# Optimization experiments

Hardware: AMD Instinct MI355X
Metric: run time of the kernel (lower is better)

## Reference

```python
import jax, jax.numpy as jnp
import numpy as np

D = 1024
H = 16
HD = D // H
FF = 4096
B = 4
S = 1024
EPS = 1e-5


def layer_norm(x, g, b):
    mu = jnp.mean(x, axis=-1, keepdims=True)
    var = jnp.mean(jnp.square(x - mu), axis=-1, keepdims=True)
    return (x - mu) * jax.lax.rsqrt(var + EPS) * g + b


def setup_inputs() -> dict:
    key = jax.random.key(0)
    ks = jax.random.split(key, 16)
    s = 0.02
    return {
        "src": jax.random.normal(ks[0], (B, S, D), jnp.float32),
        "attn_bias": jax.random.normal(ks[1], (H, S, S), jnp.float32),
        "Wqkv": jax.random.normal(ks[2], (3 * D, D), jnp.float32) * s,
        "bqkv": jnp.zeros((3 * D,), jnp.float32),
        "Wo": jax.random.normal(ks[3], (D, D), jnp.float32) * s,
        "bo": jnp.zeros((D,), jnp.float32),
        "g1": jnp.ones((D,), jnp.float32),
        "b1n": jnp.zeros((D,), jnp.float32),
        "g2": jnp.ones((D,), jnp.float32),
        "b2n": jnp.zeros((D,), jnp.float32),
        "W1": jax.random.normal(ks[4], (FF, D), jnp.float32) * s,
        "b1": jnp.zeros((FF,), jnp.float32),
        "W2": jax.random.normal(ks[5], (D, FF), jnp.float32) * s,
        "b2": jnp.zeros((D,), jnp.float32),
    }


def reference(src, attn_bias, Wqkv, bqkv, Wo, bo, g1, b1n, g2, b2n, W1, b1, W2, b2):
    bsz, seq, _ = src.shape
    qkv = src @ Wqkv.T + bqkv                      # [B,S,3D]
    q, k, v = jnp.split(qkv, 3, axis=-1)
    q = q.reshape(bsz, seq, H, HD)
    k = k.reshape(bsz, seq, H, HD)
    v = v.reshape(bsz, seq, H, HD)
    scores = jnp.einsum('bthd,bshd->bhts', q, k) / np.sqrt(HD).astype(np.float32)
    scores = scores + attn_bias[None]              # 3D bias broadcast over batch
    w = jax.nn.softmax(scores, axis=-1)
    ctx = jnp.einsum('bhts,bshd->bthd', w, v).reshape(bsz, seq, D)
    attn_out = ctx @ Wo.T + bo
    x = layer_norm(src + attn_out, g1, b1n)
    ff = (jax.nn.gelu(x @ W1.T + b1, approximate=False)) @ W2.T + b2
    return layer_norm(x + ff, g2, b2n)
```

## Files before the change

kernel.cpp:

```cpp
#include <hip/hip_runtime.h>
#include <cstdint>

typedef unsigned short u16;
typedef __bf16 bf16x8 __attribute__((ext_vector_type(8)));
typedef float f32x4 __attribute__((ext_vector_type(4)));
typedef unsigned short u16x8 __attribute__((ext_vector_type(8)));
typedef unsigned short u16x4 __attribute__((ext_vector_type(4)));

__device__ __forceinline__ u16 f2b(float f) {
  union { float f; unsigned u; } x; x.f = f;
  unsigned r = (x.u + 0x7FFFu + ((x.u >> 16) & 1u)) >> 16;
  return (u16)r;
}
__device__ __forceinline__ float b2f(u16 v) {
  union { unsigned u; float f; } x; x.u = (unsigned)v << 16; return x.f;
}

__device__ __forceinline__ void gload_lds16(const void* g, void* l) {
  __builtin_amdgcn_global_load_lds(
      (__attribute__((address_space(1))) void*)(uintptr_t)g,
      (__attribute__((address_space(3))) void*)(uintptr_t)l, 16, 0, 0);
}

struct CastArgs {
  const float* in[5];
  u16* out[5];
  int cum[6];
};
__global__ void cast_multi(CastArgs a) {
  const int i = blockIdx.x * 256 + threadIdx.x;
  int r = 0;
#pragma unroll
  for (int k = 1; k < 5; ++k) r += (i >= a.cum[k]);
  const int local = i - a.cum[r];
  const float4 v = *(const float4*)(a.in[r] + (size_t)local * 4);
  u16x4 o = {f2b(v.x), f2b(v.y), f2b(v.z), f2b(v.w)};
  *(u16x4*)(a.out[r] + (size_t)local * 4) = o;
}

template<bool GELU_ACT, bool WRITE_VT>
__global__ void gemm_nt(const u16* __restrict__ A, const u16* __restrict__ Bw,
                        const float* __restrict__ bias, u16* __restrict__ Cb,
                        u16* __restrict__ Vt, int M, int N, int K) {
  __shared__ u16 As[2][128 * 32];
  __shared__ u16 Bs[2][128 * 32];
  const int tid = threadIdx.x;
  const int lane = tid & 63, wid = tid >> 6;
  const int bm = blockIdx.y * 128, bn = blockIdx.x * 128;
  const int wm = wid >> 1, wn = wid & 1;
  const int r = lane & 15, g = lane >> 4;
  const int s4 = (r >> 1) & 3;

  auto stage = [&](int buf, int k0) {
#pragma unroll
    for (int i = 0; i < 2; ++i) {
      const int c = tid + i * 256;
      const int row = c >> 2, ch = c & 3;
      const int gs = ch ^ ((row >> 1) & 3);
      gload_lds16(A + (size_t)(bm + row) * K + k0 + gs * 8, &As[buf][c * 8]);
      gload_lds16(Bw + (size_t)(bn + row) * K + k0 + gs * 8, &Bs[buf][c * 8]);
    }
  };

  f32x4 acc[4][4] = {};
  stage(0, 0);
  __syncthreads();
  const int nk = K >> 5;
  int cur = 0;
  for (int kt = 0; kt < nk; ++kt) {
    if (kt + 1 < nk) stage(cur ^ 1, (kt + 1) * 32);
    bf16x8 af[4], bfr[4];
#pragma unroll
    for (int m = 0; m < 4; ++m)
      af[m] = *(const bf16x8*)&As[cur][(wm * 64 + m * 16 + r) * 32 + (g ^ s4) * 8];
#pragma unroll
    for (int n = 0; n < 4; ++n)
      bfr[n] = *(const bf16x8*)&Bs[cur][(wn * 64 + n * 16 + r) * 32 + (g ^ s4) * 8];
#pragma unroll
    for (int m = 0; m < 4; ++m)
#pragma unroll
      for (int n = 0; n < 4; ++n)
        acc[m][n] = __builtin_amdgcn_mfma_f32_16x16x32_bf16(af[m], bfr[n], acc[m][n], 0, 0, 0);
    __syncthreads();
    cur ^= 1;
  }
#pragma unroll
  for (int m = 0; m < 4; ++m) {
    const int row0 = bm + wm * 64 + m * 16 + g * 4;
#pragma unroll
    for (int n = 0; n < 4; ++n) {
      const int col = bn + wn * 64 + n * 16 + r;
      const float bv = bias[col];
      if (WRITE_VT && col >= 2048) {
        const int hv = col - 2048;
        const int bb = row0 >> 10, s0 = row0 & 1023;
        u16x4 ov;
#pragma unroll
        for (int j = 0; j < 4; ++j) ov[j] = f2b(acc[m][n][j] + bv);
        *(u16x4*)(Vt + (((size_t)(bb * 16 + (hv >> 6))) * 64 + (hv & 63)) * 1024 + s0) = ov;
      } else {
#pragma unroll
        for (int j = 0; j < 4; ++j) {
          float v = acc[m][n][j] + bv;
          if (GELU_ACT) v = 0.5f * v * (1.f + erff(v * 0.70710678118654752f));
          Cb[(size_t)(row0 + j) * N + col] = f2b(v);
        }
      }
    }
  }
}

__global__ void gemm_nt_splitk(const u16* __restrict__ A, const u16* __restrict__ Bw,
                               float* __restrict__ parts, int M, int N, int K, int Kc) {
  __shared__ u16 As[2][128 * 32];
  __shared__ u16 Bs[2][128 * 32];
  const int tid = threadIdx.x;
  const int lane = tid & 63, wid = tid >> 6;
  const int bm = blockIdx.y * 128, bn = blockIdx.x * 128;
  const int kbase = blockIdx.z * Kc;
  const int wm = wid >> 1, wn = wid & 1;
  const int r = lane & 15, g = lane >> 4;
  const int s4 = (r >> 1) & 3;

  auto stage = [&](int buf, int k0) {
#pragma unroll
    for (int i = 0; i < 2; ++i) {
      const int c = tid + i * 256;
      const int row = c >> 2, ch = c & 3;
      const int gs = ch ^ ((row >> 1) & 3);
      gload_lds16(A + (size_t)(bm + row) * K + k0 + gs * 8, &As[buf][c * 8]);
      gload_lds16(Bw + (size_t)(bn + row) * K + k0 + gs * 8, &Bs[buf][c * 8]);
    }
  };

  f32x4 acc[4][4] = {};
  stage(0, kbase);
  __syncthreads();
  const int nk = Kc >> 5;
  int cur = 0;
  for (int kt = 0; kt < nk; ++kt) {
    if (kt + 1 < nk) stage(cur ^ 1, kbase + (kt + 1) * 32);
    bf16x8 af[4], bfr[4];
#pragma unroll
    for (int m = 0; m < 4; ++m)
      af[m] = *(const bf16x8*)&As[cur][(wm * 64 + m * 16 + r) * 32 + (g ^ s4) * 8];
#pragma unroll
    for (int n = 0; n < 4; ++n)
      bfr[n] = *(const bf16x8*)&Bs[cur][(wn * 64 + n * 16 + r) * 32 + (g ^ s4) * 8];
#pragma unroll
    for (int m = 0; m < 4; ++m)
#pragma unroll
      for (int n = 0; n < 4; ++n)
        acc[m][n] = __builtin_amdgcn_mfma_f32_16x16x32_bf16(af[m], bfr[n], acc[m][n], 0, 0, 0);
    __syncthreads();
    cur ^= 1;
  }
  float* Cp = parts + (size_t)blockIdx.z * M * N;
#pragma unroll
  for (int m = 0; m < 4; ++m) {
    const int row0 = bm + wm * 64 + m * 16 + g * 4;
#pragma unroll
    for (int n = 0; n < 4; ++n) {
      const int col = bn + wn * 64 + n * 16 + r;
#pragma unroll
      for (int j = 0; j < 4; ++j)
        Cp[(size_t)(row0 + j) * N + col] = acc[m][n][j];
    }
  }
}

__global__ __launch_bounds__(256) void attn_kernel(
    const u16* __restrict__ qkv, const u16* __restrict__ Vt,
    const float* __restrict__ bias, u16* __restrict__ ctx) {
  const int yy = blockIdx.y;
  const int h = yy >> 2, b = yy & 3;
  const int q0 = blockIdx.x * 32;
  const int tid = threadIdx.x;
  const int lane = tid & 63, wid = tid >> 6;
  const int r = lane & 15, g = lane >> 4;
  const int bh = b * 16 + h;

  __shared__ __align__(16) u16 PB[2][16 * 1024];

  const size_t qb0 = (size_t)(b * 1024 + q0 + r) * 3072 + h * 64;
  const size_t qb1 = (size_t)(b * 1024 + q0 + 16 + r) * 3072 + h * 64;
  const bf16x8 aq00 = *(const bf16x8*)(qkv + qb0 + g * 8);
  const bf16x8 aq01 = *(const bf16x8*)(qkv + qb0 + 32 + g * 8);
  const bf16x8 aq10 = *(const bf16x8*)(qkv + qb1 + g * 8);
  const bf16x8 aq11 = *(const bf16x8*)(qkv + qb1 + 32 + g * 8);

  const int n0 = wid * 256;
  const float* brow0 = bias + ((size_t)h * 1024 + q0 + r) * 1024;
  const float* brow1 = brow0 + 16 * 1024;

#pragma unroll 4
  for (int nt = 0; nt < 16; ++nt) {
    const int key = n0 + nt * 16 + r;
    const size_t kbase = (size_t)(b * 1024 + key) * 3072 + 1024 + h * 64;
    const bf16x8 bk0 = *(const bf16x8*)(qkv + kbase + g * 8);
    const bf16x8 bk1 = *(const bf16x8*)(qkv + kbase + 32 + g * 8);
    const int col = n0 + nt * 16 + g * 4;
    const float4 bb0 = *(const float4*)(brow0 + col);
    const float4 bb1 = *(const float4*)(brow1 + col);
    f32x4 a0 = {0.f, 0.f, 0.f, 0.f}, a1 = {0.f, 0.f, 0.f, 0.f};
    a0 = __builtin_amdgcn_mfma_f32_16x16x32_bf16(bk0, aq00, a0, 0, 0, 0);
    a1 = __builtin_amdgcn_mfma_f32_16x16x32_bf16(bk0, aq10, a1, 0, 0, 0);
    a0 = __builtin_amdgcn_mfma_f32_16x16x32_bf16(bk1, aq01, a0, 0, 0, 0);
    a1 = __builtin_amdgcn_mfma_f32_16x16x32_bf16(bk1, aq11, a1, 0, 0, 0);
    const int idx = r * 1024 + (col ^ ((r & 15) << 3));
    u16x4 o0 = {f2b(fmaf(a0[0], 0.125f, bb0.x)), f2b(fmaf(a0[1], 0.125f, bb0.y)),
                f2b(fmaf(a0[2], 0.125f, bb0.z)), f2b(fmaf(a0[3], 0.125f, bb0.w))};
    u16x4 o1 = {f2b(fmaf(a1[0], 0.125f, bb1.x)), f2b(fmaf(a1[1], 0.125f, bb1.y)),
                f2b(fmaf(a1[2], 0.125f, bb1.z)), f2b(fmaf(a1[3], 0.125f, bb1.w))};
    *(u16x4*)&PB[0][idx] = o0;
    *(u16x4*)&PB[1][idx] = o1;
  }
  __syncthreads();

#pragma unroll
  for (int tr = 0; tr < 8; ++tr) {
    const int t = tr & 1, rr = tr >> 1;
    const int row = wid * 4 + rr;
    const int swz = (row & 15) << 3;
    u16* prow = &PB[t][row * 1024];
    const int c0 = lane * 16;
    const u16x8 v0 = *(const u16x8*)&prow[c0 ^ swz];
    const u16x8 v1 = *(const u16x8*)&prow[(c0 + 8) ^ swz];
    float f[16];
#pragma unroll
    for (int k = 0; k < 8; ++k) { f[k] = b2f(v0[k]); f[8 + k] = b2f(v1[k]); }
    float m = f[0];
#pragma unroll
    for (int k = 1; k < 16; ++k) m = fmaxf(m, f[k]);
    m = fmaxf(m, __shfl_xor(m, 1));  m = fmaxf(m, __shfl_xor(m, 2));
    m = fmaxf(m, __shfl_xor(m, 4));  m = fmaxf(m, __shfl_xor(m, 8));
    m = fmaxf(m, __shfl_xor(m, 16)); m = fmaxf(m, __shfl_xor(m, 32));
    float s = 0.f;
#pragma unroll
    for (int k = 0; k < 16; ++k) { f[k] = __expf(f[k] - m); s += f[k]; }
    s += __shfl_xor(s, 1);  s += __shfl_xor(s, 2);
    s += __shfl_xor(s, 4);  s += __shfl_xor(s, 8);
    s += __shfl_xor(s, 16); s += __shfl_xor(s, 32);
    const float inv = 1.f / s;
    u16x8 o0, o1;
#pragma unroll
    for (int k = 0; k < 8; ++k) {
      o0[k] = f2b(f[k] * inv);
      o1[k] = f2b(f[8 + k] * inv);
    }
    *(u16x8*)&prow[c0 ^ swz] = o0;
    *(u16x8*)&prow[(c0 + 8) ^ swz] = o1;
  }
  __syncthreads();

  f32x4 oa = {0.f, 0.f, 0.f, 0.f}, ob = {0.f, 0.f, 0.f, 0.f};
  const u16* vrow = Vt + ((size_t)bh * 64 + wid * 16 + r) * 1024;
#pragma unroll 4
  for (int ks = 0; ks < 32; ++ks) {
    const int off = (ks * 32 + g * 8) ^ ((r & 15) << 3);
    const bf16x8 vb = *(const bf16x8*)(vrow + ks * 32 + g * 8);
    const bf16x8 pa0 = *(const bf16x8*)&PB[0][r * 1024 + off];
    const bf16x8 pa1 = *(const bf16x8*)&PB[1][r * 1024 + off];
    oa = __builtin_amdgcn_mfma_f32_16x16x32_bf16(pa0, vb, oa, 0, 0, 0);
    ob = __builtin_amdgcn_mfma_f32_16x16x32_bf16(pa1, vb, ob, 0, 0, 0);
  }
#pragma unroll
  for (int j = 0; j < 4; ++j) {
    ctx[(size_t)(b * 1024 + q0 + g * 4 + j) * 1024 + h * 64 + wid * 16 + r] = f2b(oa[j]);
    ctx[(size_t)(b * 1024 + q0 + 16 + g * 4 + j) * 1024 + h * 64 + wid * 16 + r] = f2b(ob[j]);
  }
}

template<int NP>
__global__ void ln_sum_kernel(const float* __restrict__ parts,
                              const float* __restrict__ resid,
                              const float* __restrict__ cbias,
                              const float* __restrict__ gw, const float* __restrict__ bw,
                              float* __restrict__ outf, u16* __restrict__ outb) {
  const int row = blockIdx.x, tid = threadIdx.x;
  const size_t off = (size_t)row * 1024 + tid * 4;
  float4 v = *(const float4*)(resid + off);
  const float4 cb = *(const float4*)(cbias + tid * 4);
  v.x += cb.x; v.y += cb.y; v.z += cb.z; v.w += cb.w;
#pragma unroll
  for (int p = 0; p < NP; ++p) {
    const float4 a = *(const float4*)(parts + (size_t)p * 4096 * 1024 + off);
    v.x += a.x; v.y += a.y; v.z += a.z; v.w += a.w;
  }
  float s = v.x + v.y + v.z + v.w;
  float q = v.x * v.x + v.y * v.y + v.z * v.z + v.w * v.w;
#pragma unroll
  for (int m = 32; m >= 1; m >>= 1) { s += __shfl_xor(s, m); q += __shfl_xor(q, m); }
  __shared__ float rs[4], rq[4];
  if ((tid & 63) == 0) { rs[tid >> 6] = s; rq[tid >> 6] = q; }
  __syncthreads();
  s = rs[0] + rs[1] + rs[2] + rs[3];
  q = rq[0] + rq[1] + rq[2] + rq[3];
  const float mu = s * (1.f / 1024.f);
  const float inv = rsqrtf(q * (1.f / 1024.f) - mu * mu + 1e-5f);
  const float4 g4 = *(const float4*)(gw + tid * 4);
  const float4 b4 = *(const float4*)(bw + tid * 4);
  float4 o;
  o.x = (v.x - mu) * inv * g4.x + b4.x;
  o.y = (v.y - mu) * inv * g4.y + b4.y;
  o.z = (v.z - mu) * inv * g4.z + b4.z;
  o.w = (v.w - mu) * inv * g4.w + b4.w;
  if (outf) *(float4*)(outf + off) = o;
  if (outb) {
    u16x4 ob = {f2b(o.x), f2b(o.y), f2b(o.z), f2b(o.w)};
    *(u16x4*)(outb + off) = ob;
  }
}

extern "C" void kernel_launch(void* const* d_in, const int* in_sizes, int n_in,
                              void* d_out, int out_size, void* d_ws, size_t ws_size,
                              hipStream_t stream) {
  (void)in_sizes; (void)n_in; (void)out_size; (void)ws_size;
  const float* src   = (const float*)d_in[0];
  const float* abias = (const float*)d_in[1];
  const float* Wqkv  = (const float*)d_in[2];
  const float* bqkv  = (const float*)d_in[3];
  const float* Wo    = (const float*)d_in[4];
  const float* bo    = (const float*)d_in[5];
  const float* g1    = (const float*)d_in[6];
  const float* b1n   = (const float*)d_in[7];
  const float* g2    = (const float*)d_in[8];
  const float* b2n   = (const float*)d_in[9];
  const float* W1    = (const float*)d_in[10];
  const float* b1    = (const float*)d_in[11];
  const float* W2    = (const float*)d_in[12];
  const float* b2    = (const float*)d_in[13];
  float* out = (float*)d_out;

  char* ws = (char*)d_ws;
  const size_t MB = 1024 * 1024;
  u16* srcb  = (u16*)(ws + 0 * MB);
  u16* ctxb  = (u16*)(ws + 0 * MB);
  u16* xb    = (u16*)(ws + 0 * MB);
  u16* Wqkvb = (u16*)(ws + 8 * MB);
  u16* Wob   = (u16*)(ws + 14 * MB);
  float* xf  = (float*)(ws + 8 * MB);
  u16* W2b   = (u16*)(ws + 24 * MB);
  u16* qkvb  = (u16*)(ws + 32 * MB);
  u16* Vt    = (u16*)(ws + 56 * MB);
  u16* hb    = (u16*)(ws + 32 * MB);
  float* parts = (float*)(ws + 64 * MB);
  u16* W1b   = (u16*)(ws + 96 * MB);

  CastArgs ca;
  ca.in[0] = src;  ca.out[0] = srcb;
  ca.in[1] = Wqkv; ca.out[1] = Wqkvb;
  ca.in[2] = Wo;   ca.out[2] = Wob;
  ca.in[3] = W1;   ca.out[3] = W1b;
  ca.in[4] = W2;   ca.out[4] = W2b;
  ca.cum[0] = 0;
  ca.cum[1] = 1048576;
  ca.cum[2] = 1048576 + 786432;
  ca.cum[3] = 1048576 + 786432 + 262144;
  ca.cum[4] = 1048576 + 786432 + 262144 + 1048576;
  ca.cum[5] = 4194304;
  cast_multi<<<4194304 / 256, 256, 0, stream>>>(ca);

  gemm_nt<false, true><<<dim3(3072 / 128, 4096 / 128), 256, 0, stream>>>(
      srcb, Wqkvb, bqkv, qkvb, Vt, 4096, 3072, 1024);
  attn_kernel<<<dim3(32, 64), 256, 0, stream>>>(qkvb, Vt, abias, ctxb);
  gemm_nt_splitk<<<dim3(1024 / 128, 4096 / 128, 2), 256, 0, stream>>>(
      ctxb, Wob, parts, 4096, 1024, 1024, 512);
  ln_sum_kernel<2><<<4096, 256, 0, stream>>>(parts, src, bo, g1, b1n, xf, xb);
  gemm_nt<true, false><<<dim3(4096 / 128, 4096 / 128), 256, 0, stream>>>(
      xb, W1b, b1, hb, nullptr, 4096, 4096, 1024);
  gemm_nt_splitk<<<dim3(1024 / 128, 4096 / 128, 2), 256, 0, stream>>>(
      hb, W2b, parts, 4096, 1024, 4096, 2048);
  ln_sum_kernel<2><<<4096, 256, 0, stream>>>(parts, xf, b2, g2, b2n, out, nullptr);
}
```

Before: 296.6 us.

## Remap attention blocks for XCD-local bias reuse and add bias in softmax pass

```diff
diff --git a/kernel.cpp b/kernel.cpp
--- a/kernel.cpp
+++ b/kernel.cpp
@@ -172,9 +172,12 @@
 __global__ __launch_bounds__(256) void attn_kernel(
     const u16* __restrict__ qkv, const u16* __restrict__ Vt,
     const float* __restrict__ bias, u16* __restrict__ ctx) {
-  const int yy = blockIdx.y;
-  const int h = yy >> 2, b = yy & 3;
-  const int q0 = blockIdx.x * 32;
+  const int fid = blockIdx.x;
+  const int xcd = fid & 7, slot = fid >> 3;
+  const int G = xcd * 64 + (slot >> 2);
+  const int b = slot & 3;
+  const int h = G >> 5;
+  const int q0 = (G & 31) * 32;
   const int tid = threadIdx.x;
   const int lane = tid & 63, wid = tid >> 6;
   const int r = lane & 15, g = lane >> 4;
@@ -190,8 +193,6 @@
   const bf16x8 aq11 = *(const bf16x8*)(qkv + qb1 + 32 + g * 8);
 
   const int n0 = wid * 256;
-  const float* brow0 = bias + ((size_t)h * 1024 + q0 + r) * 1024;
-  const float* brow1 = brow0 + 16 * 1024;
 
 #pragma unroll 4
   for (int nt = 0; nt < 16; ++nt) {
@@ -199,19 +200,17 @@
     const size_t kbase = (size_t)(b * 1024 + key) * 3072 + 1024 + h * 64;
     const bf16x8 bk0 = *(const bf16x8*)(qkv + kbase + g * 8);
     const bf16x8 bk1 = *(const bf16x8*)(qkv + kbase + 32 + g * 8);
-    const int col = n0 + nt * 16 + g * 4;
-    const float4 bb0 = *(const float4*)(brow0 + col);
-    const float4 bb1 = *(const float4*)(brow1 + col);
     f32x4 a0 = {0.f, 0.f, 0.f, 0.f}, a1 = {0.f, 0.f, 0.f, 0.f};
     a0 = __builtin_amdgcn_mfma_f32_16x16x32_bf16(bk0, aq00, a0, 0, 0, 0);
     a1 = __builtin_amdgcn_mfma_f32_16x16x32_bf16(bk0, aq10, a1, 0, 0, 0);
     a0 = __builtin_amdgcn_mfma_f32_16x16x32_bf16(bk1, aq01, a0, 0, 0, 0);
     a1 = __builtin_amdgcn_mfma_f32_16x16x32_bf16(bk1, aq11, a1, 0, 0, 0);
+    const int col = n0 + nt * 16 + g * 4;
     const int idx = r * 1024 + (col ^ ((r & 15) << 3));
-    u16x4 o0 = {f2b(fmaf(a0[0], 0.125f, bb0.x)), f2b(fmaf(a0[1], 0.125f, bb0.y)),
-                f2b(fmaf(a0[2], 0.125f, bb0.z)), f2b(fmaf(a0[3], 0.125f, bb0.w))};
-    u16x4 o1 = {f2b(fmaf(a1[0], 0.125f, bb1.x)), f2b(fmaf(a1[1], 0.125f, bb1.y)),
-                f2b(fmaf(a1[2], 0.125f, bb1.z)), f2b(fmaf(a1[3], 0.125f, bb1.w))};
+    u16x4 o0 = {f2b(a0[0] * 0.125f), f2b(a0[1] * 0.125f),
+                f2b(a0[2] * 0.125f), f2b(a0[3] * 0.125f)};
+    u16x4 o1 = {f2b(a1[0] * 0.125f), f2b(a1[1] * 0.125f),
+                f2b(a1[2] * 0.125f), f2b(a1[3] * 0.125f)};
     *(u16x4*)&PB[0][idx] = o0;
     *(u16x4*)&PB[1][idx] = o1;
   }
@@ -223,12 +222,21 @@
     const int row = wid * 4 + rr;
     const int swz = (row & 15) << 3;
     u16* prow = &PB[t][row * 1024];
+    const float* brow = bias + ((size_t)h * 1024 + q0 + t * 16 + row) * 1024;
     const int c0 = lane * 16;
+    float bb[16];
+    *(float4*)&bb[0]  = *(const float4*)(brow + c0);
+    *(float4*)&bb[4]  = *(const float4*)(brow + c0 + 4);
+    *(float4*)&bb[8]  = *(const float4*)(brow + c0 + 8);
+    *(float4*)&bb[12] = *(const float4*)(brow + c0 + 12);
     const u16x8 v0 = *(const u16x8*)&prow[c0 ^ swz];
     const u16x8 v1 = *(const u16x8*)&prow[(c0 + 8) ^ swz];
     float f[16];
 #pragma unroll
-    for (int k = 0; k < 8; ++k) { f[k] = b2f(v0[k]); f[8 + k] = b2f(v1[k]); }
+    for (int k = 0; k < 8; ++k) {
+      f[k]     = b2f(v0[k]) + bb[k];
+      f[8 + k] = b2f(v1[k]) + bb[8 + k];
+    }
     float m = f[0];
 #pragma unroll
     for (int k = 1; k < 16; ++k) m = fmaxf(m, f[k]);
@@ -271,15 +279,21 @@
   }
 }
 
-template<int NP>
+template<int NP, bool RESID_BF16>
 __global__ void ln_sum_kernel(const float* __restrict__ parts,
-                              const float* __restrict__ resid,
+                              const void* __restrict__ resid,
                               const float* __restrict__ cbias,
                               const float* __restrict__ gw, const float* __restrict__ bw,
                               float* __restrict__ outf, u16* __restrict__ outb) {
   const int row = blockIdx.x, tid = threadIdx.x;
   const size_t off = (size_t)row * 1024 + tid * 4;
-  float4 v = *(const float4*)(resid + off);
+  float4 v;
+  if (RESID_BF16) {
+    const u16x4 rb = *(const u16x4*)((const u16*)resid + off);
+    v.x = b2f(rb[0]); v.y = b2f(rb[1]); v.z = b2f(rb[2]); v.w = b2f(rb[3]);
+  } else {
+    v = *(const float4*)((const float*)resid + off);
+  }
   const float4 cb = *(const float4*)(cbias + tid * 4);
   v.x += cb.x; v.y += cb.y; v.z += cb.z; v.w += cb.w;
 #pragma unroll
@@ -339,7 +353,6 @@
   u16* xb    = (u16*)(ws + 0 * MB);
   u16* Wqkvb = (u16*)(ws + 8 * MB);
   u16* Wob   = (u16*)(ws + 14 * MB);
-  float* xf  = (float*)(ws + 8 * MB);
   u16* W2b   = (u16*)(ws + 24 * MB);
   u16* qkvb  = (u16*)(ws + 32 * MB);
   u16* Vt    = (u16*)(ws + 56 * MB);
@@ -363,13 +376,15 @@
 
   gemm_nt<false, true><<<dim3(3072 / 128, 4096 / 128), 256, 0, stream>>>(
       srcb, Wqkvb, bqkv, qkvb, Vt, 4096, 3072, 1024);
-  attn_kernel<<<dim3(32, 64), 256, 0, stream>>>(qkvb, Vt, abias, ctxb);
+  attn_kernel<<<2048, 256, 0, stream>>>(qkvb, Vt, abias, ctxb);
   gemm_nt_splitk<<<dim3(1024 / 128, 4096 / 128, 2), 256, 0, stream>>>(
       ctxb, Wob, parts, 4096, 1024, 1024, 512);
-  ln_sum_kernel<2><<<4096, 256, 0, stream>>>(parts, src, bo, g1, b1n, xf, xb);
+  ln_sum_kernel<2, false><<<4096, 256, 0, stream>>>(
+      parts, src, bo, g1, b1n, nullptr, xb);
   gemm_nt<true, false><<<dim3(4096 / 128, 4096 / 128), 256, 0, stream>>>(
       xb, W1b, b1, hb, nullptr, 4096, 4096, 1024);
   gemm_nt_splitk<<<dim3(1024 / 128, 4096 / 128, 2), 256, 0, stream>>>(
       hb, W2b, parts, 4096, 1024, 4096, 2048);
-  ln_sum_kernel<2><<<4096, 256, 0, stream>>>(parts, xf, b2, g2, b2n, out, nullptr);
-}
+  ln_sum_kernel<2, true><<<4096, 256, 0, stream>>>(
+      parts, xb, b2, g2, b2n, out, nullptr);
+}
```

Result: faster. 284.6 us (-4.0%).
